# Kernel optimization log

Hardware: AMD Instinct MI355X
Metric: run time of the kernel (lower is better)

## Reference

```python
import jax, jax.numpy as jnp
import numpy as np

NUM_ROUTING = 3


def squash(s, axis):
    # v = |s|^2/(1+|s|^2) * s/|s|  (eq. 1 of the CapsNet paper)
    mag_sq = jnp.sum(s * s, axis=axis, keepdims=True)
    mag = jnp.sqrt(mag_sq)
    return mag_sq / (1.0 + mag_sq) * (s / mag)


def setup_inputs() -> dict:
    key = jax.random.key(0)
    k1, k2 = jax.random.split(key)
    B, I, C, U, S = 256, 8, 1152, 10, 16
    x = jax.random.normal(k1, (B, I, C), dtype=jnp.float32)
    weight = jax.random.normal(k2, (1, C, U, S, I), dtype=jnp.float32)
    return {"x": x, "weight": weight}


def reference(x, weight):
    # x: [B, in_unit, in_channel]; weight: [1, C, U, S, I]
    B = x.shape[0]
    C, U = weight.shape[1], weight.shape[2]
    x_t = jnp.transpose(x, (0, 2, 1))  # [B, C, I]
    # u_hat[b,c,u,s] = sum_i W[0,c,u,s,i] * x_t[b,c,i]
    u_hat = jnp.einsum('cusi,bci->bcus', weight[0], x_t)  # [B, C, U, S]

    b_ij = jnp.zeros((1, C, U, 1), dtype=u_hat.dtype)
    # s_j = (c_ij * u_hat).sum(dim=0): c_ij is batch-independent, so
    # precompute the batch-sum once instead of re-broadcasting each iter.
    u_sum = jnp.sum(u_hat, axis=0, keepdims=True)  # [1, C, U, S]

    v_j = None
    for _ in range(NUM_ROUTING):
        c_ij = jax.nn.softmax(b_ij, axis=2)          # [1, C, U, 1]
        s_j = c_ij * u_sum                           # [1, C, U, S]
        v_j = squash(s_j, axis=3)                    # [1, C, U, S]
        # agreement: mean over batch of <u_hat[b,c,u,:], v_j[0,c,u,:]>
        u_vj1 = jnp.einsum('bcus,cus->cu', u_hat, v_j[0]) / B  # [C, U]
        b_ij = b_ij + u_vj1[None, :, :, None]
    return v_j[0]  # squeeze -> [C, U, S]
```

## Files before the change

### kernel.cpp

```cpp
#include <hip/hip_runtime.h>

#define B_DIM 256
#define I_DIM 8
#define C_DIM 1152
#define U_DIM 10
#define S_DIM 16
#define ROW (I_DIM * C_DIM)

__global__ __launch_bounds__(256) void capsule_fused(
    const float* __restrict__ x, const float* __restrict__ W,
    float* __restrict__ out) {
  __shared__ float4 fold[256];
  __shared__ float xs_lds[16][I_DIM];

  const int tid = threadIdx.x;
  const int c0 = blockIdx.x * 16;
  const int c_local = tid >> 4;
  const int s = tid & 15;
  const int c = c0 + c_local;

  const float4* wp =
      (const float4*)(W + (size_t)c * (U_DIM * S_DIM * I_DIM) + s * I_DIM);
  float4 wreg[U_DIM][2];
#pragma unroll
  for (int u = 0; u < U_DIM; ++u) {
    wreg[u][0] = wp[u * (S_DIM * I_DIM / 4)];
    wreg[u][1] = wp[u * (S_DIM * I_DIM / 4) + 1];
  }

  {
    const int b8 = tid >> 5;
    const int i = (tid >> 2) & 7;
    const int cq = tid & 3;
    const float* p = x + (size_t)(b8 * 32) * ROW + i * C_DIM + c0 + cq * 4;
    float4 acc = {0.f, 0.f, 0.f, 0.f};
#pragma unroll 16
    for (int j = 0; j < 32; ++j) {
      const float4 v = *(const float4*)(p + (size_t)j * ROW);
      acc.x += v.x; acc.y += v.y; acc.z += v.z; acc.w += v.w;
    }
    fold[tid] = acc;
  }
  __syncthreads();
  if (tid < 32) {
    float4 a = fold[tid];
#pragma unroll
    for (int k = 1; k < 8; ++k) {
      const float4 v = fold[k * 32 + tid];
      a.x += v.x; a.y += v.y; a.z += v.z; a.w += v.w;
    }
    const int i = tid >> 2, cq = tid & 3;
    xs_lds[cq * 4 + 0][i] = a.x;
    xs_lds[cq * 4 + 1][i] = a.y;
    xs_lds[cq * 4 + 2][i] = a.z;
    xs_lds[cq * 4 + 3][i] = a.w;
  }
  __syncthreads();

  float xs[I_DIM];
#pragma unroll
  for (int i = 0; i < I_DIM; ++i) xs[i] = xs_lds[c_local][i];

  float us[U_DIM];
#pragma unroll
  for (int u = 0; u < U_DIM; ++u) {
    const float4 w0 = wreg[u][0], w1 = wreg[u][1];
    us[u] = w0.x * xs[0] + w0.y * xs[1] + w0.z * xs[2] + w0.w * xs[3] +
            w1.x * xs[4] + w1.y * xs[5] + w1.z * xs[6] + w1.w * xs[7];
  }

  float bij[U_DIM];
  float v[U_DIM];

#pragma unroll
  for (int u = 0; u < U_DIM; ++u) {
    const float sj = 0.1f * us[u];
    float msq = sj * sj;
#pragma unroll
    for (int w = 1; w < 16; w <<= 1) msq += __shfl_xor(msq, w);
    const float mag = sqrtf(msq);
    const float v0 = (msq / (1.f + msq)) * (sj / mag);
    v[u] = v0;
    float a = us[u] * v0;
#pragma unroll
    for (int w = 1; w < 16; w <<= 1) a += __shfl_xor(a, w);
    bij[u] = a * (1.f / (float)B_DIM);
  }

#pragma unroll
  for (int it = 1; it < 3; ++it) {
    float m = bij[0];
#pragma unroll
    for (int u = 1; u < U_DIM; ++u) m = fmaxf(m, bij[u]);
    float e[U_DIM];
    float sum = 0.f;
#pragma unroll
    for (int u = 0; u < U_DIM; ++u) { e[u] = __expf(bij[u] - m); sum += e[u]; }
    const float inv = 1.f / sum;

#pragma unroll
    for (int u = 0; u < U_DIM; ++u) {
      const float sj = e[u] * inv * us[u];
      float msq = sj * sj;
#pragma unroll
      for (int w = 1; w < 16; w <<= 1) msq += __shfl_xor(msq, w);
      const float mag = sqrtf(msq);
      const float vv = (msq / (1.f + msq)) * (sj / mag);
      v[u] = vv;
      if (it < 2) {
        float a = us[u] * vv;
#pragma unroll
        for (int w = 1; w < 16; w <<= 1) a += __shfl_xor(a, w);
        bij[u] += a * (1.f / (float)B_DIM);
      }
    }
  }

#pragma unroll
  for (int u = 0; u < U_DIM; ++u)
    out[(size_t)c * (U_DIM * S_DIM) + u * S_DIM + s] = v[u];
}

extern "C" void kernel_launch(void* const* d_in, const int* in_sizes, int n_in,
                              void* d_out, int out_size, void* d_ws, size_t ws_size,
                              hipStream_t stream) {
  const float* x = (const float*)d_in[0];
  const float* W = (const float*)d_in[1];
  float* out = (float*)d_out;
  (void)d_ws; (void)ws_size;

  capsule_fused<<<dim3(C_DIM / 16), 256, 0, stream>>>(x, W, out);
}
```

Baseline: 78.30 us.

## Shrink per-block channel tile to 4 to launch more blocks for the x batch-sum

Each block now handles 4 capsule channels instead of 16, so the grid grows from 72 to 288 blocks. The batch reduction of x is repartitioned so all 256 threads each sum 8 batch rows of one float4, followed by a 32-way LDS fold. This aims to spread the memory-bound x reduction across more CUs. The cost is that only 64 threads per block do the routing math, and each x load is a single 16-byte float4 per row, which may reduce coalescing efficiency.

```diff
diff --git a/kernel.cpp b/kernel.cpp
--- a/kernel.cpp
+++ b/kernel.cpp
@@ -10,53 +10,54 @@
 __global__ __launch_bounds__(256) void capsule_fused(
     const float* __restrict__ x, const float* __restrict__ W,
     float* __restrict__ out) {
-  __shared__ float4 fold[256];
-  __shared__ float xs_lds[16][I_DIM];
+  __shared__ float4 fold[32][I_DIM];
+  __shared__ float xs_lds[4][I_DIM];
 
   const int tid = threadIdx.x;
-  const int c0 = blockIdx.x * 16;
+  const int c0 = blockIdx.x * 4;
   const int c_local = tid >> 4;
   const int s = tid & 15;
-  const int c = c0 + c_local;
 
-  const float4* wp =
-      (const float4*)(W + (size_t)c * (U_DIM * S_DIM * I_DIM) + s * I_DIM);
   float4 wreg[U_DIM][2];
+  if (tid < 64) {
+    const float4* wp = (const float4*)(W +
+        (size_t)(c0 + c_local) * (U_DIM * S_DIM * I_DIM) + s * I_DIM);
 #pragma unroll
-  for (int u = 0; u < U_DIM; ++u) {
-    wreg[u][0] = wp[u * (S_DIM * I_DIM / 4)];
-    wreg[u][1] = wp[u * (S_DIM * I_DIM / 4) + 1];
+    for (int u = 0; u < U_DIM; ++u) {
+      wreg[u][0] = wp[u * (S_DIM * I_DIM / 4)];
+      wreg[u][1] = wp[u * (S_DIM * I_DIM / 4) + 1];
+    }
   }
 
   {
-    const int b8 = tid >> 5;
-    const int i = (tid >> 2) & 7;
-    const int cq = tid & 3;
-    const float* p = x + (size_t)(b8 * 32) * ROW + i * C_DIM + c0 + cq * 4;
+    const int bp = tid >> 3;
+    const int i = tid & 7;
+    const float* p = x + (size_t)(bp * 8) * ROW + i * C_DIM + c0;
     float4 acc = {0.f, 0.f, 0.f, 0.f};
-#pragma unroll 16
-    for (int j = 0; j < 32; ++j) {
+#pragma unroll
+    for (int j = 0; j < 8; ++j) {
       const float4 v = *(const float4*)(p + (size_t)j * ROW);
       acc.x += v.x; acc.y += v.y; acc.z += v.z; acc.w += v.w;
     }
-    fold[tid] = acc;
+    fold[bp][i] = acc;
   }
   __syncthreads();
-  if (tid < 32) {
-    float4 a = fold[tid];
+  if (tid < 8) {
+    float4 a = fold[0][tid];
 #pragma unroll
-    for (int k = 1; k < 8; ++k) {
-      const float4 v = fold[k * 32 + tid];
+    for (int k = 1; k < 32; ++k) {
+      const float4 v = fold[k][tid];
       a.x += v.x; a.y += v.y; a.z += v.z; a.w += v.w;
     }
-    const int i = tid >> 2, cq = tid & 3;
-    xs_lds[cq * 4 + 0][i] = a.x;
-    xs_lds[cq * 4 + 1][i] = a.y;
-    xs_lds[cq * 4 + 2][i] = a.z;
-    xs_lds[cq * 4 + 3][i] = a.w;
+    xs_lds[0][tid] = a.x;
+    xs_lds[1][tid] = a.y;
+    xs_lds[2][tid] = a.z;
+    xs_lds[3][tid] = a.w;
   }
   __syncthreads();
+  if (tid >= 64) return;
 
+  const int c = c0 + c_local;
   float xs[I_DIM];
 #pragma unroll
   for (int i = 0; i < I_DIM; ++i) xs[i] = xs_lds[c_local][i];
@@ -129,5 +130,5 @@
   float* out = (float*)d_out;
   (void)d_ws; (void)ws_size;
 
-  capsule_fused<<<dim3(C_DIM / 16), 256, 0, stream>>>(x, W, out);
+  capsule_fused<<<dim3(C_DIM / 4), 256, 0, stream>>>(x, W, out);
 }
```

After: 80.12 us. +2.3%, slower.
